# Performance work log

Hardware: AMD Instinct MI355X
Metric: run time of the kernel (lower is better)

The kernel has to match this reference:

```python
import jax, jax.numpy as jnp
import numpy as np

NUM_HEADS = 16

def setup_inputs() -> dict:
    key = jax.random.key(0)
    ks = jax.random.split(key, 4)
    D = 1024
    x = jax.random.normal(ks[0], (2, 8192, D), dtype=jnp.float32)
    s = 1.0 / np.sqrt(D)
    Wqkv = jax.random.normal(ks[1], (D, 3 * D), dtype=jnp.float32) * s
    Wq = jax.random.normal(ks[2], (D, D), dtype=jnp.float32) * s
    Wproj = jax.random.normal(ks[3], (D, D), dtype=jnp.float32) * s
    return {
        "x": x,
        "Wqkv": Wqkv, "bqkv": jnp.zeros((3 * D,), jnp.float32),
        "Wq": Wq, "bq": jnp.zeros((D,), jnp.float32),
        "Wproj": Wproj, "bproj": jnp.zeros((D,), jnp.float32),
        "num_anchor_tokens": 1024,
    }

def reference(x, Wqkv, bqkv, Wq, bq, Wproj, bproj, num_anchor_tokens):
    B, S, D = x.shape
    H = NUM_HEADS
    hd = D // H
    A = num_anchor_tokens
    scale = 1.0 / jnp.sqrt(jnp.float32(hd))

    anchors = x[:, :A, :]          # (B, A, D)
    queries = x[:, A:, :]          # (B, Sq, D)
    Sq = S - A

    # Anchor QKV projection: (B, A, 3, H, hd)
    aqkv = (anchors @ Wqkv + bqkv).reshape(B, A, 3, H, hd)
    aqkv = jnp.transpose(aqkv, (2, 0, 3, 1, 4))   # (3, B, H, A, hd)
    aq, ak, av = aqkv[0], aqkv[1], aqkv[2]

    # Query-token Q projection: (B, H, Sq, hd)
    qq = (queries @ Wq + bq).reshape(B, Sq, H, hd)
    qq = jnp.transpose(qq, (0, 2, 1, 3))

    q = jnp.concatenate([aq, qq], axis=2)         # (B, H, S, hd)

    # All queries attend only to anchor keys/values
    scores = jnp.einsum('bhqd,bhkd->bhqk', q, ak) * scale   # (B, H, S, A)
    attn = jax.nn.softmax(scores, axis=-1)
    out = jnp.einsum('bhqk,bhkd->bhqd', attn, av)           # (B, H, S, hd)

    out = jnp.transpose(out, (0, 2, 1, 3)).reshape(B, S, D)
    return out @ Wproj + bproj
```

## Files before the change

### kernel.cpp

```cpp
#include <hip/hip_runtime.h>
#include <cstdint>

#define B_ 2
#define S_ 8192
#define D_ 1024
#define H_ 16
#define HD_ 64
#define A_ 1024
#define SQ_ 7168

#define QSCALE 0.18033688011112042f

typedef unsigned short ushort_t;
typedef unsigned int uint_t;
typedef __bf16 bf16x8 __attribute__((ext_vector_type(8)));
typedef __bf16 bf16x4 __attribute__((ext_vector_type(4)));
typedef float floatx4 __attribute__((ext_vector_type(4)));
typedef ushort_t ushort8 __attribute__((ext_vector_type(8)));
typedef uint_t uint2v __attribute__((ext_vector_type(2)));

__device__ __forceinline__ ushort_t f2bf(float f) {
  uint_t u = __builtin_bit_cast(uint_t, f);
  u += 0x7fffu + ((u >> 16) & 1u);
  return (ushort_t)(u >> 16);
}
__device__ __forceinline__ ushort_t f2bf_c(float f) {
  __bf16 h = (__bf16)f;
  return __builtin_bit_cast(ushort_t, h);
}

__device__ __forceinline__ void glds16(const ushort_t* g, ushort_t* l) {
  __builtin_amdgcn_global_load_lds(
      (const __attribute__((address_space(1))) void*)g,
      (__attribute__((address_space(3))) void*)l, 16, 0, 0);
}

__global__ __launch_bounds__(256) void cvt_x(const float* __restrict__ x,
                                             ushort_t* __restrict__ xb) {
  int i = (blockIdx.x * 256 + threadIdx.x) * 8;
  float4 a = *(const float4*)(x + i);
  float4 b = *(const float4*)(x + i + 4);
  ushort8 o;
  o[0] = f2bf_c(a.x); o[1] = f2bf_c(a.y); o[2] = f2bf_c(a.z); o[3] = f2bf_c(a.w);
  o[4] = f2bf_c(b.x); o[5] = f2bf_c(b.y); o[6] = f2bf_c(b.z); o[7] = f2bf_c(b.w);
  *(ushort8*)(xb + i) = o;
}

__global__ __launch_bounds__(256) void cvt_w_all(
    const float* __restrict__ Wqkv, const float* __restrict__ Wq,
    const float* __restrict__ Wproj, ushort_t* __restrict__ wqkvT,
    ushort_t* __restrict__ wqT, ushort_t* __restrict__ wprojT) {
  __shared__ float t[32][33];
  const int z = blockIdx.z;
  const float* W;
  ushort_t* WT;
  int stride, colofs;
  if (z < 3)      { W = Wqkv;  WT = wqkvT + (size_t)z * 1024 * 1024; stride = 3072; colofs = z * 1024; }
  else if (z == 3){ W = Wq;    WT = wqT;    stride = 1024; colofs = 0; }
  else            { W = Wproj; WT = wprojT; stride = 1024; colofs = 0; }
  int n0 = blockIdx.x * 32, k0 = blockIdx.y * 32;
  int tx = threadIdx.x, ty = threadIdx.y;
  #pragma unroll
  for (int i = ty; i < 32; i += 8)
    t[i][tx] = W[(uint64_t)(k0 + i) * stride + colofs + n0 + tx];
  __syncthreads();
  #pragma unroll
  for (int i = ty; i < 32; i += 8)
    WT[(uint64_t)(n0 + i) * 1024 + k0 + tx] = f2bf_c(t[tx][i]);
}

template <int MODE>
__global__ __launch_bounds__(256) void gemm_bt(
    const ushort_t* __restrict__ Abase, const ushort_t* __restrict__ WT,
    const float* __restrict__ bias,
    ushort_t* __restrict__ Qb, ushort_t* __restrict__ Kb,
    ushort_t* __restrict__ Vb, float* __restrict__ outf) {
  __shared__ __align__(16) ushort_t At[128 * 32];
  __shared__ __align__(16) ushort_t Bt[128 * 32];
  const int t = threadIdx.x;
  const int lane = t & 63;
  const int quad = lane >> 4, ln = lane & 15;
  const int wave = t >> 6;
  const int wm = wave & 1, wn = wave >> 1;
  const int m0 = blockIdx.x * 128, n0 = blockIdx.y * 128;

  const int r0 = t >> 2, seg = t & 3;
  auto maprow = [&](int gm) -> int {
    if (MODE == 0) { int b = gm >> 10; int a = gm & 1023; return b * S_ + a; }
    if (MODE == 1) { int b = (gm >= SQ_) ? 1 : 0; int sq = gm - b * SQ_; return b * S_ + A_ + sq; }
    return gm;
  };
  const ushort_t* arow0 = Abase + (uint64_t)maprow(m0 + r0) * 1024;
  const ushort_t* arow1 = Abase + (uint64_t)maprow(m0 + 64 + r0) * 1024;
  const ushort_t* brow0 = WT + (uint64_t)(n0 + r0) * 1024;
  const ushort_t* brow1 = WT + (uint64_t)(n0 + 64 + r0) * 1024;
  ushort_t* At_lo = (ushort_t*)((char*)At + wave * 1024);
  ushort_t* At_hi = (ushort_t*)((char*)At + 4096 + wave * 1024);
  ushort_t* Bt_lo = (ushort_t*)((char*)Bt + wave * 1024);
  ushort_t* Bt_hi = (ushort_t*)((char*)Bt + 4096 + wave * 1024);

  floatx4 acc[4][4];
  #pragma unroll
  for (int i = 0; i < 4; ++i)
    #pragma unroll
    for (int j = 0; j < 4; ++j) acc[i][j] = (floatx4)0.0f;

  for (int k0 = 0; k0 < 1024; k0 += 32) {
    __syncthreads();
    glds16(arow0 + k0 + seg * 8, At_lo);
    glds16(arow1 + k0 + seg * 8, At_hi);
    glds16(brow0 + k0 + seg * 8, Bt_lo);
    glds16(brow1 + k0 + seg * 8, Bt_hi);
    __syncthreads();
    bf16x8 af[4], bfr[4];
    #pragma unroll
    for (int i = 0; i < 4; ++i)
      af[i] = *(const bf16x8*)&At[(wm * 64 + i * 16 + ln) * 32 + quad * 8];
    #pragma unroll
    for (int j = 0; j < 4; ++j)
      bfr[j] = *(const bf16x8*)&Bt[(wn * 64 + j * 16 + ln) * 32 + quad * 8];
    #pragma unroll
    for (int i = 0; i < 4; ++i)
      #pragma unroll
      for (int j = 0; j < 4; ++j)
        acc[i][j] = __builtin_amdgcn_mfma_f32_16x16x32_bf16(af[i], bfr[j], acc[i][j], 0, 0, 0);
  }

  #pragma unroll
  for (int i = 0; i < 4; ++i) {
    #pragma unroll
    for (int j = 0; j < 4; ++j) {
      #pragma unroll
      for (int r = 0; r < 4; ++r) {
        int gm = m0 + wm * 64 + i * 16 + quad * 4 + r;
        int gn = n0 + wn * 64 + j * 16 + ln;
        float v = acc[i][j][r] + bias[gn];
        if (MODE == 2) {
          outf[(uint64_t)gm * 1024 + gn] = v;
        } else if (MODE == 0) {
          int b = gm >> 10, a = gm & 1023;
          int which = gn >> 10, h = (gn >> 6) & 15, d = gn & 63;
          if (which == 0)
            Qb[((uint64_t)(b * H_ + h) * S_ + a) * HD_ + d] = f2bf_c(v * QSCALE);
          else if (which == 1)
            Kb[((uint64_t)(b * H_ + h) * A_ + a) * HD_ + d] = f2bf_c(v);
          else
            Vb[((uint64_t)(b * H_ + h) * HD_ + d) * A_ + a] = f2bf_c(v);
        } else {
          int b = (gm >= SQ_) ? 1 : 0; int sq = gm - b * SQ_;
          int h = gn >> 6, d = gn & 63;
          Qb[((uint64_t)(b * H_ + h) * S_ + (A_ + sq)) * HD_ + d] = f2bf_c(v * QSCALE);
        }
      }
    }
  }
}

__global__ __launch_bounds__(256) void attn_mfma(const ushort_t* __restrict__ Qb,
                                                 const ushort_t* __restrict__ Kb,
                                                 const ushort_t* __restrict__ Vb,
                                                 ushort_t* __restrict__ Ob) {
  __shared__ __align__(16) ushort_t Ks[64 * 72];
  __shared__ __align__(16) ushort_t Vt[80 * 72];
  __shared__ __align__(16) ushort_t Ps[128 * 72];
  const int t = threadIdx.x;
  const int lane = t & 63;
  const int quad = lane >> 4, ln = lane & 15;
  const int wave = t >> 6;
  const int wm = wave & 1, wn = wave >> 1;
  const int bh = blockIdx.y;
  const int b = bh >> 4, h = bh & 15;
  const int m0 = blockIdx.x * 128;

  bf16x8 qf[4][2];
  {
    const ushort_t* qbase = Qb + ((uint64_t)bh * S_ + m0 + wn * 64 + ln) * HD_ + quad * 8;
    #pragma unroll
    for (int j = 0; j < 4; ++j)
      #pragma unroll
      for (int ks = 0; ks < 2; ++ks)
        qf[j][ks] = *(const bf16x8*)(qbase + (uint64_t)(j * 16) * HD_ + ks * 32);
  }
  if (t < 64) Vt[64 * 72 + t] = 0x3F80;

  floatx4 oacc[2][5];
  #pragma unroll
  for (int i = 0; i < 2; ++i)
    #pragma unroll
    for (int j = 0; j < 5; ++j) oacc[i][j] = (floatx4)0.0f;

  const ushort_t* kcbase = Kb + (uint64_t)bh * A_ * HD_;
  const ushort_t* vcbase = Vb + (uint64_t)bh * HD_ * A_;
  const int srow = t >> 2, sseg = t & 3;

  for (int kc = 0; kc < 16; ++kc) {
    const ushort_t* kg = kcbase + (uint64_t)(kc * 64 + srow) * 64 + sseg * 16;
    const ushort_t* vg = vcbase + (uint64_t)srow * A_ + kc * 64 + sseg * 16;
    ushort8 k0 = *(const ushort8*)kg;
    ushort8 k1 = *(const ushort8*)(kg + 8);
    ushort8 v0 = *(const ushort8*)vg;
    ushort8 v1 = *(const ushort8*)(vg + 8);
    __syncthreads();
    *(ushort8*)&Ks[srow * 72 + sseg * 16] = k0;
    *(ushort8*)&Ks[srow * 72 + sseg * 16 + 8] = k1;
    *(ushort8*)&Vt[srow * 72 + sseg * 16] = v0;
    *(ushort8*)&Vt[srow * 72 + sseg * 16 + 8] = v1;
    __syncthreads();

    floatx4 sacc[2][4];
    #pragma unroll
    for (int i = 0; i < 2; ++i)
      #pragma unroll
      for (int j = 0; j < 4; ++j) sacc[i][j] = (floatx4)0.0f;
    __builtin_amdgcn_s_setprio(1);
    #pragma unroll
    for (int ks = 0; ks < 2; ++ks) {
      bf16x8 kf[2];
      #pragma unroll
      for (int i = 0; i < 2; ++i)
        kf[i] = *(const bf16x8*)&Ks[(wm * 32 + i * 16 + ln) * 72 + ks * 32 + quad * 8];
      #pragma unroll
      for (int i = 0; i < 2; ++i)
        #pragma unroll
        for (int j = 0; j < 4; ++j)
          sacc[i][j] = __builtin_amdgcn_mfma_f32_16x16x32_bf16(kf[i], qf[j][ks], sacc[i][j], 0, 0, 0);
    }
    __builtin_amdgcn_s_setprio(0);
    #pragma unroll
    for (int i = 0; i < 2; ++i)
      #pragma unroll
      for (int j = 0; j < 4; ++j) {
        float p0 = __builtin_amdgcn_exp2f(sacc[i][j][0]);
        float p1 = __builtin_amdgcn_exp2f(sacc[i][j][1]);
        float p2 = __builtin_amdgcn_exp2f(sacc[i][j][2]);
        float p3 = __builtin_amdgcn_exp2f(sacc[i][j][3]);
        bf16x4 pv;
        pv[0] = (__bf16)p0; pv[1] = (__bf16)p1;
        pv[2] = (__bf16)p2; pv[3] = (__bf16)p3;
        int q = wn * 64 + j * 16 + ln;
        int key = wm * 32 + i * 16 + quad * 4;
        *(bf16x4*)&Ps[q * 72 + key] = pv;
      }
    __syncthreads();

    __builtin_amdgcn_s_setprio(1);
    #pragma unroll
    for (int ks = 0; ks < 2; ++ks) {
      bf16x8 af[2];
      #pragma unroll
      for (int i2 = 0; i2 < 2; ++i2)
        af[i2] = *(const bf16x8*)&Ps[(wave * 32 + i2 * 16 + ln) * 72 + ks * 32 + quad * 8];
      bf16x8 bv[5];
      #pragma unroll
      for (int j = 0; j < 5; ++j)
        bv[j] = *(const bf16x8*)&Vt[(j * 16 + ln) * 72 + ks * 32 + quad * 8];
      #pragma unroll
      for (int i2 = 0; i2 < 2; ++i2)
        #pragma unroll
        for (int j = 0; j < 5; ++j)
          oacc[i2][j] = __builtin_amdgcn_mfma_f32_16x16x32_bf16(af[i2], bv[j], oacc[i2][j], 0, 0, 0);
    }
    __builtin_amdgcn_s_setprio(0);
  }

  #pragma unroll
  for (int i2 = 0; i2 < 2; ++i2) {
    #pragma unroll
    for (int r = 0; r < 4; ++r) {
      float lsum = __shfl(oacc[i2][4][r], lane & 48);
      float inv = 1.0f / lsum;
      int qrow = m0 + wave * 32 + i2 * 16 + quad * 4 + r;
      ushort_t* op = Ob + ((uint64_t)b * S_ + qrow) * D_ + h * HD_;
      #pragma unroll
      for (int j = 0; j < 4; ++j)
        op[j * 16 + ln] = f2bf_c(oacc[i2][j][r] * inv);
    }
  }
}

extern "C" void kernel_launch(void* const* d_in, const int* in_sizes, int n_in,
                              void* d_out, int out_size, void* d_ws, size_t ws_size,
                              hipStream_t stream) {
  (void)in_sizes; (void)n_in; (void)out_size; (void)ws_size;
  const float* x     = (const float*)d_in[0];
  const float* Wqkv  = (const float*)d_in[1];
  const float* bqkv  = (const float*)d_in[2];
  const float* Wq    = (const float*)d_in[3];
  const float* bq    = (const float*)d_in[4];
  const float* Wproj = (const float*)d_in[5];
  const float* bproj = (const float*)d_in[6];
  float* out = (float*)d_out;

  char* ws = (char*)d_ws;
  ushort_t* xb     = (ushort_t*)ws; ws += (size_t)B_ * S_ * D_ * 2;
  ushort_t* wqkvT  = (ushort_t*)ws; ws += (size_t)3 * D_ * D_ * 2;
  ushort_t* wqT    = (ushort_t*)ws; ws += (size_t)D_ * D_ * 2;
  ushort_t* wprojT = (ushort_t*)ws; ws += (size_t)D_ * D_ * 2;
  ushort_t* Qb     = (ushort_t*)ws; ws += (size_t)B_ * H_ * S_ * HD_ * 2;
  ushort_t* Kb     = (ushort_t*)ws; ws += (size_t)B_ * H_ * A_ * HD_ * 2;
  ushort_t* Vb     = (ushort_t*)ws; ws += (size_t)B_ * H_ * A_ * HD_ * 2;
  ushort_t* Ob     = (ushort_t*)ws;

  cvt_x<<<dim3((B_ * S_ * D_) / (256 * 8)), dim3(256), 0, stream>>>(x, xb);
  cvt_w_all<<<dim3(32, 32, 5), dim3(32, 8), 0, stream>>>(
      Wqkv, Wq, Wproj, wqkvT, wqT, wprojT);

  gemm_bt<0><<<dim3((B_ * A_) / 128, 3072 / 128), dim3(256), 0, stream>>>(
      xb, wqkvT, bqkv, Qb, Kb, Vb, nullptr);
  gemm_bt<1><<<dim3((B_ * SQ_) / 128, 1024 / 128), dim3(256), 0, stream>>>(
      xb, wqT, bq, Qb, nullptr, nullptr, nullptr);
  attn_mfma<<<dim3(S_ / 128, B_ * H_), dim3(256), 0, stream>>>(Qb, Kb, Vb, Ob);
  gemm_bt<2><<<dim3((B_ * S_) / 128, 1024 / 128), dim3(256), 0, stream>>>(
      Ob, wprojT, bproj, nullptr, nullptr, nullptr, out);
}
```

Baseline: 373.4 us.

## Merge anchor QKV and query-Q GEMMs into one launch with swizzled block order

Replaces the two projection GEMM launches (anchor QKV and query-token Q) with a single kernel of 1280 blocks. Each block derives from its linear id whether it does the QKV or the Q tile. The block index is remapped (interleaved by 8) in both this kernel and the output projection GEMM, so that concurrently running blocks share A/B tiles in cache. This removes one launch and the tail underutilisation of the small anchor GEMM, and is meant to improve L2 reuse. The cost is a runtime branch on the tile type and division/modulo index math per block.

```diff
diff --git a/kernel.cpp b/kernel.cpp
--- a/kernel.cpp
+++ b/kernel.cpp
@@ -17,13 +17,7 @@
 typedef __bf16 bf16x4 __attribute__((ext_vector_type(4)));
 typedef float floatx4 __attribute__((ext_vector_type(4)));
 typedef ushort_t ushort8 __attribute__((ext_vector_type(8)));
-typedef uint_t uint2v __attribute__((ext_vector_type(2)));
-
-__device__ __forceinline__ ushort_t f2bf(float f) {
-  uint_t u = __builtin_bit_cast(uint_t, f);
-  u += 0x7fffu + ((u >> 16) & 1u);
-  return (ushort_t)(u >> 16);
-}
+
 __device__ __forceinline__ ushort_t f2bf_c(float f) {
   __bf16 h = (__bf16)f;
   return __builtin_bit_cast(ushort_t, h);
@@ -69,12 +63,11 @@
     WT[(uint64_t)(n0 + i) * 1024 + k0 + tx] = f2bf_c(t[tx][i]);
 }
 
-template <int MODE>
-__global__ __launch_bounds__(256) void gemm_bt(
-    const ushort_t* __restrict__ Abase, const ushort_t* __restrict__ WT,
-    const float* __restrict__ bias,
-    ushort_t* __restrict__ Qb, ushort_t* __restrict__ Kb,
-    ushort_t* __restrict__ Vb, float* __restrict__ outf) {
+__global__ __launch_bounds__(256) void gemm_qkvq(
+    const ushort_t* __restrict__ xb, const ushort_t* __restrict__ wqkvT,
+    const ushort_t* __restrict__ wqT, const float* __restrict__ bqkv,
+    const float* __restrict__ bq, ushort_t* __restrict__ Qb,
+    ushort_t* __restrict__ Kb, ushort_t* __restrict__ Vb) {
   __shared__ __align__(16) ushort_t At[128 * 32];
   __shared__ __align__(16) ushort_t Bt[128 * 32];
   const int t = threadIdx.x;
@@ -82,16 +75,25 @@
   const int quad = lane >> 4, ln = lane & 15;
   const int wave = t >> 6;
   const int wm = wave & 1, wn = wave >> 1;
-  const int m0 = blockIdx.x * 128, n0 = blockIdx.y * 128;
+
+  const int lin = blockIdx.x;
+  const int id = (lin & 7) * 160 + (lin >> 3);
+  const bool is0 = id < 384;
+  int bx, by;
+  if (is0) { bx = id & 15; by = id >> 4; }
+  else     { int i2 = id - 384; bx = i2 % 112; by = i2 / 112; }
+  const int m0 = bx * 128, n0 = by * 128;
+  const ushort_t* WT = is0 ? wqkvT : wqT;
+  const float* bias = is0 ? bqkv : bq;
 
   const int r0 = t >> 2, seg = t & 3;
   auto maprow = [&](int gm) -> int {
-    if (MODE == 0) { int b = gm >> 10; int a = gm & 1023; return b * S_ + a; }
-    if (MODE == 1) { int b = (gm >= SQ_) ? 1 : 0; int sq = gm - b * SQ_; return b * S_ + A_ + sq; }
-    return gm;
+    if (is0) return (gm >> 10) * S_ + (gm & 1023);
+    int bb = (gm >= SQ_) ? 1 : 0;
+    return bb * S_ + A_ + (gm - bb * SQ_);
   };
-  const ushort_t* arow0 = Abase + (uint64_t)maprow(m0 + r0) * 1024;
-  const ushort_t* arow1 = Abase + (uint64_t)maprow(m0 + 64 + r0) * 1024;
+  const ushort_t* arow0 = xb + (uint64_t)maprow(m0 + r0) * 1024;
+  const ushort_t* arow1 = xb + (uint64_t)maprow(m0 + 64 + r0) * 1024;
   const ushort_t* brow0 = WT + (uint64_t)(n0 + r0) * 1024;
   const ushort_t* brow1 = WT + (uint64_t)(n0 + 64 + r0) * 1024;
   ushort_t* At_lo = (ushort_t*)((char*)At + wave * 1024);
@@ -135,9 +137,7 @@
         int gm = m0 + wm * 64 + i * 16 + quad * 4 + r;
         int gn = n0 + wn * 64 + j * 16 + ln;
         float v = acc[i][j][r] + bias[gn];
-        if (MODE == 2) {
-          outf[(uint64_t)gm * 1024 + gn] = v;
-        } else if (MODE == 0) {
+        if (is0) {
           int b = gm >> 10, a = gm & 1023;
           int which = gn >> 10, h = (gn >> 6) & 15, d = gn & 63;
           if (which == 0)
@@ -151,6 +151,72 @@
           int h = gn >> 6, d = gn & 63;
           Qb[((uint64_t)(b * H_ + h) * S_ + (A_ + sq)) * HD_ + d] = f2bf_c(v * QSCALE);
         }
+      }
+    }
+  }
+}
+
+__global__ __launch_bounds__(256) void gemm_proj(
+    const ushort_t* __restrict__ Ob, const ushort_t* __restrict__ WT,
+    const float* __restrict__ bias, float* __restrict__ outf) {
+  __shared__ __align__(16) ushort_t At[128 * 32];
+  __shared__ __align__(16) ushort_t Bt[128 * 32];
+  const int t = threadIdx.x;
+  const int lane = t & 63;
+  const int quad = lane >> 4, ln = lane & 15;
+  const int wave = t >> 6;
+  const int wm = wave & 1, wn = wave >> 1;
+
+  const int lin = blockIdx.x + (int)blockIdx.y * 128;
+  const int swz = (lin & 7) * 128 + (lin >> 3);
+  const int m0 = (swz & 127) * 128, n0 = (swz >> 7) * 128;
+
+  const int r0 = t >> 2, seg = t & 3;
+  const ushort_t* arow0 = Ob + (uint64_t)(m0 + r0) * 1024;
+  const ushort_t* arow1 = Ob + (uint64_t)(m0 + 64 + r0) * 1024;
+  const ushort_t* brow0 = WT + (uint64_t)(n0 + r0) * 1024;
+  const ushort_t* brow1 = WT + (uint64_t)(n0 + 64 + r0) * 1024;
+  ushort_t* At_lo = (ushort_t*)((char*)At + wave * 1024);
+  ushort_t* At_hi = (ushort_t*)((char*)At + 4096 + wave * 1024);
+  ushort_t* Bt_lo = (ushort_t*)((char*)Bt + wave * 1024);
+  ushort_t* Bt_hi = (ushort_t*)((char*)Bt + 4096 + wave * 1024);
+
+  floatx4 acc[4][4];
+  #pragma unroll
+  for (int i = 0; i < 4; ++i)
+    #pragma unroll
+    for (int j = 0; j < 4; ++j) acc[i][j] = (floatx4)0.0f;
+
+  for (int k0 = 0; k0 < 1024; k0 += 32) {
+    __syncthreads();
+    glds16(arow0 + k0 + seg * 8, At_lo);
+    glds16(arow1 + k0 + seg * 8, At_hi);
+    glds16(brow0 + k0 + seg * 8, Bt_lo);
+    glds16(brow1 + k0 + seg * 8, Bt_hi);
+    __syncthreads();
+    bf16x8 af[4], bfr[4];
+    #pragma unroll
+    for (int i = 0; i < 4; ++i)
+      af[i] = *(const bf16x8*)&At[(wm * 64 + i * 16 + ln) * 32 + quad * 8];
+    #pragma unroll
+    for (int j = 0; j < 4; ++j)
+      bfr[j] = *(const bf16x8*)&Bt[(wn * 64 + j * 16 + ln) * 32 + quad * 8];
+    #pragma unroll
+    for (int i = 0; i < 4; ++i)
+      #pragma unroll
+      for (int j = 0; j < 4; ++j)
+        acc[i][j] = __builtin_amdgcn_mfma_f32_16x16x32_bf16(af[i], bfr[j], acc[i][j], 0, 0, 0);
+  }
+
+  #pragma unroll
+  for (int i = 0; i < 4; ++i) {
+    #pragma unroll
+    for (int j = 0; j < 4; ++j) {
+      #pragma unroll
+      for (int r = 0; r < 4; ++r) {
+        int gm = m0 + wm * 64 + i * 16 + quad * 4 + r;
+        int gn = n0 + wn * 64 + j * 16 + ln;
+        outf[(uint64_t)gm * 1024 + gn] = acc[i][j][r] + bias[gn];
       }
     }
   }
@@ -305,11 +371,8 @@
   cvt_w_all<<<dim3(32, 32, 5), dim3(32, 8), 0, stream>>>(
       Wqkv, Wq, Wproj, wqkvT, wqT, wprojT);
 
-  gemm_bt<0><<<dim3((B_ * A_) / 128, 3072 / 128), dim3(256), 0, stream>>>(
-      xb, wqkvT, bqkv, Qb, Kb, Vb, nullptr);
-  gemm_bt<1><<<dim3((B_ * SQ_) / 128, 1024 / 128), dim3(256), 0, stream>>>(
-      xb, wqT, bq, Qb, nullptr, nullptr, nullptr);
+  gemm_qkvq<<<dim3(1280), dim3(256), 0, stream>>>(
+      xb, wqkvT, wqT, bqkv, bq, Qb, Kb, Vb);
   attn_mfma<<<dim3(S_ / 128, B_ * H_), dim3(256), 0, stream>>>(Qb, Kb, Vb, Ob);
-  gemm_bt<2><<<dim3((B_ * S_) / 128, 1024 / 128), dim3(256), 0, stream>>>(
-      Ob, wprojT, bproj, nullptr, nullptr, nullptr, out);
-}
+  gemm_proj<<<dim3(128, 8), dim3(256), 0, stream>>>(Ob, wprojT, bproj, out);
+}
```

New measurement: 379.4 us. No clear change (+1.6%).
